# Kernel tuning notes

Hardware: AMD Instinct MI355X
Metric: run time of the kernel (lower is better)

Reference implementation:

```python
import jax, jax.numpy as jnp
import numpy as np

V, E, H = 50257, 512, 1024  # vocab, embed_dim, hidden_dim
B, S = 64, 2048             # batch, src_len


def setup_inputs() -> dict:
    key = jax.random.key(0)
    ks = jax.random.split(key, 16)
    sc = 0.02
    emb = jax.random.normal(ks[0], (V, E), jnp.float32) * sc
    emb = emb.at[0].set(0.0)  # padding_idx=0
    return {
        "x": jax.random.randint(ks[1], (B, 1), 0, V),
        "hidden": jax.random.normal(ks[2], (1, B, H), jnp.float32),
        "cell": jax.random.normal(ks[3], (1, B, H), jnp.float32),
        "encoder_outputs": jax.random.normal(ks[4], (B, S, H), jnp.float32),
        "emb": emb,
        "Wa_w": jax.random.normal(ks[5], (H, H), jnp.float32) * sc,
        "Wa_b": jnp.zeros((H,), jnp.float32),
        "Ua_w": jax.random.normal(ks[6], (H, H), jnp.float32) * sc,
        "Ua_b": jnp.zeros((H,), jnp.float32),
        "va_w": jax.random.normal(ks[7], (1, H), jnp.float32) * sc,
        "va_b": jnp.zeros((1,), jnp.float32),
        "Wih": jax.random.normal(ks[8], (4 * H, E + H), jnp.float32) * sc,
        "Whh": jax.random.normal(ks[9], (4 * H, H), jnp.float32) * sc,
        "bih": jnp.zeros((4 * H,), jnp.float32),
        "bhh": jnp.zeros((4 * H,), jnp.float32),
        "fc_w": jax.random.normal(ks[10], (V, H), jnp.float32) * sc,
        "fc_b": jnp.zeros((V,), jnp.float32),
    }


def reference(x, hidden, cell, encoder_outputs, emb, Wa_w, Wa_b, Ua_w, Ua_b,
              va_w, va_b, Wih, Whh, bih, bhh, fc_w, fc_b):
    # Embedding lookup: [B,1] -> [B,E]
    embedded = emb[x[:, 0]]
    # Bahdanau additive attention
    s_t = hidden[-1]                                          # [B,H]
    proj_s = jnp.einsum('bh,oh->bo', s_t, Wa_w) + Wa_b        # [B,H]
    proj_e = jnp.einsum('bsh,oh->bso', encoder_outputs, Ua_w) + Ua_b  # [B,S,H]
    e = jnp.tanh(proj_s[:, None, :] + proj_e)                 # [B,S,H]
    scores = jnp.einsum('bsh,h->bs', e, va_w[0]) + va_b[0]    # [B,S]
    attn = jax.nn.softmax(scores, axis=1)                     # [B,S]
    context = jnp.einsum('bs,bsh->bh', attn, encoder_outputs)  # [B,H]
    # Single-step LSTM (torch gate order: i, f, g, o)
    lstm_in = jnp.concatenate([embedded, context], axis=1)    # [B,E+H]
    gates = lstm_in @ Wih.T + bih + s_t @ Whh.T + bhh         # [B,4H]
    i, f, g, o = jnp.split(gates, 4, axis=1)
    i, f, o = jax.nn.sigmoid(i), jax.nn.sigmoid(f), jax.nn.sigmoid(o)
    g = jnp.tanh(g)
    c_new = f * cell[-1] + i * g
    h_new = o * jnp.tanh(c_new)
    predictions = (h_new @ fc_w.T + fc_b)[:, None, :]          # [B,1,V]
    return predictions, h_new[None], c_new[None]
```

## Files before the change

### kernel.cpp

```cpp
#include <hip/hip_runtime.h>
#include <hip/hip_bf16.h>

#define V_ 50257
#define H_ 1024
#define S_ 2048

typedef float f32x4 __attribute__((ext_vector_type(4)));
typedef short s16x8 __attribute__((ext_vector_type(8)));

__device__ __forceinline__ unsigned short f2bf(float f){
  unsigned u = __builtin_bit_cast(unsigned, f);
  return (unsigned short)((u + 0x7FFFu + ((u >> 16) & 1u)) >> 16);
}
__device__ __forceinline__ unsigned cvt2(float a, float b){
  return (unsigned)f2bf(a) | ((unsigned)f2bf(b) << 16);
}
__device__ __forceinline__ float bf2f(unsigned short h){
  return __builtin_bit_cast(float, (unsigned)h << 16);
}
__device__ __forceinline__ float fast_tanh(float x){
  return 1.0f - 2.0f/(__expf(2.0f*x)+1.0f);
}
__device__ __forceinline__ float fast_sig(float x){
  return 1.0f/(1.0f+__expf(-x));
}
__device__ __forceinline__ void gld_lds16(const void* g, void* l){
  __builtin_amdgcn_global_load_lds((const __attribute__((address_space(1))) void*)g,
                                   (__attribute__((address_space(3))) void*)l, 16, 0, 0);
}

#define BAR() do { __builtin_amdgcn_sched_barrier(0); __builtin_amdgcn_s_barrier(); __builtin_amdgcn_sched_barrier(0); } while(0)
#define VMW4() asm volatile("s_waitcnt vmcnt(4)" ::: "memory")
#define VMW2() asm volatile("s_waitcnt vmcnt(2)" ::: "memory")
#define VMW0() asm volatile("s_waitcnt vmcnt(0)" ::: "memory")

__global__ __launch_bounds__(256) void k_cvt_bf16(const float* __restrict__ src,
                                                  unsigned short* __restrict__ dst, int n){
  int i = (blockIdx.x*256 + threadIdx.x)*4;
  if (i < n){
    float4 f = *(const float4*)(src + i);
    uint2 u;
    u.x = cvt2(f.x, f.y);
    u.y = cvt2(f.z, f.w);
    *(uint2*)(dst + i) = u;
  }
}

__global__ __launch_bounds__(256) void k_cvt_enc(const float* __restrict__ src,
                                                 unsigned short* __restrict__ dst){
  const size_t stride = (size_t)gridDim.x * 256;
  const float4* s4 = (const float4*)src;
  uint2* d2 = (uint2*)dst;
  for (size_t i = (size_t)blockIdx.x*256 + threadIdx.x; i < 33554432u; i += stride){
    float4 f = s4[i];
    uint2 u;
    u.x = cvt2(f.x, f.y);
    u.y = cvt2(f.z, f.w);
    d2[i] = u;
  }
}

__global__ __launch_bounds__(1024,4) void k_proje256(
    const unsigned short* __restrict__ A,
    const unsigned short* __restrict__ Bw,
    const float* __restrict__ ps,
    const float* __restrict__ Ua_b,
    const float* __restrict__ va,
    float* __restrict__ part)
{
  extern __shared__ unsigned short smem[];
  const int t = threadIdx.x;
  const int lane = t & 63, wid = t >> 6;
  const int lr = lane & 15, lk = lane >> 4;
  const int wr = wid >> 2, wc = wid & 3;

  int bid = blockIdx.x;
  int L = (bid & 7) * 256 + (bid >> 3);
  const int wgm = L >> 2, wgn = L & 3;
  const int m0 = wgm * 256, n0 = wgn * 256;

  const int srow = lane >> 3;
  const int schunk = (lane & 7) ^ srow;

  f32x4 acc[4][4] = {};
  s16x8 af[4], bfr[4];

  auto STAGE_A = [&](int slot, int kt){
    #pragma unroll
    for (int h = 0; h < 2; ++h){
      unsigned short* ldst = smem + slot*16384;
      int rb = h*128 + wid*8;
      gld_lds16(A + (size_t)(m0 + rb + srow)*1024 + kt*64 + schunk*8,
                ldst + rb*64);
    }
  };
  auto STAGE_B = [&](int slot, int kt){
    #pragma unroll
    for (int h = 0; h < 2; ++h){
      unsigned short* ldst = smem + 32768 + slot*16384;
      int rb = h*128 + wid*8;
      gld_lds16(Bw + (size_t)(n0 + rb + srow)*1024 + kt*64 + schunk*8,
                ldst + rb*64);
    }
  };

#define SUBPH(As_, Bs_, ks) do { \
    _Pragma("unroll") \
    for (int ni = 0; ni < 4; ++ni){ \
      int rl = wc*64 + ni*16 + lr; \
      bfr[ni] = *(const s16x8*)((Bs_) + rl*64 + ((((ks)*4+lk) ^ (lr&7))*8)); \
    } \
    _Pragma("unroll") \
    for (int mi = 0; mi < 4; ++mi){ \
      int rl = wr*64 + mi*16 + lr; \
      af[mi] = *(const s16x8*)((As_) + rl*64 + ((((ks)*4+lk) ^ (lr&7))*8)); \
    } \
    __builtin_amdgcn_s_setprio(1); \
    _Pragma("unroll") \
    for (int mi = 0; mi < 4; ++mi) \
      _Pragma("unroll") \
      for (int ni = 0; ni < 4; ++ni) \
        acc[mi][ni] = __builtin_amdgcn_mfma_f32_16x16x32_bf16(af[mi], bfr[ni], acc[mi][ni], 0,0,0); \
    __builtin_amdgcn_s_setprio(0); \
  } while(0)

  const unsigned short* As0 = smem;
  const unsigned short* Bs0 = smem + 32768;
  const unsigned short* As1 = smem + 16384;
  const unsigned short* Bs1 = smem + 32768 + 16384;

  STAGE_A(0, 0); STAGE_B(0, 0);
  STAGE_A(1, 1); STAGE_B(1, 1);
  VMW4(); BAR();

  for (int i = 0; i < 8; ++i){
    SUBPH(As0, Bs0, 0);
    SUBPH(As0, Bs0, 1);
    BAR();
    if (i < 7){
      STAGE_A(0, 2*i + 2);
      VMW2(); BAR();
      SUBPH(As1, Bs1, 0);
      STAGE_B(0, 2*i + 2);
      SUBPH(As1, Bs1, 1);
      BAR();
      STAGE_A(1, 2*i + 3);
      STAGE_B(1, 2*i + 3);
      VMW4(); BAR();
    } else {
      VMW0(); BAR();
      SUBPH(As1, Bs1, 0);
      SUBPH(As1, Bs1, 1);
    }
  }

  const int b = m0 >> 11;
  float psv[4], vav[4];
  #pragma unroll
  for (int ni = 0; ni < 4; ++ni){
    int n = n0 + wc*64 + ni*16 + lr;
    psv[ni] = ps[b*1024 + n] + Ua_b[n];
    vav[ni] = va[n];
  }
  #pragma unroll
  for (int mi = 0; mi < 4; ++mi){
    float p0=0.f,p1=0.f,p2=0.f,p3=0.f;
    #pragma unroll
    for (int ni = 0; ni < 4; ++ni){
      p0 += vav[ni]*fast_tanh(acc[mi][ni][0] + psv[ni]);
      p1 += vav[ni]*fast_tanh(acc[mi][ni][1] + psv[ni]);
      p2 += vav[ni]*fast_tanh(acc[mi][ni][2] + psv[ni]);
      p3 += vav[ni]*fast_tanh(acc[mi][ni][3] + psv[ni]);
    }
    #pragma unroll
    for (int off = 1; off < 16; off <<= 1){
      p0 += __shfl_xor(p0, off);
      p1 += __shfl_xor(p1, off);
      p2 += __shfl_xor(p2, off);
      p3 += __shfl_xor(p3, off);
    }
    if (lr == 0){
      int rg = m0 + wr*64 + mi*16 + lk*4;
      int slot = wgn*4 + wc;
      part[(size_t)rg*16 + slot]     = p0;
      part[(size_t)(rg+1)*16 + slot] = p1;
      part[(size_t)(rg+2)*16 + slot] = p2;
      part[(size_t)(rg+3)*16 + slot] = p3;
    }
  }
#undef SUBPH
}

__global__ __launch_bounds__(256,2) void k_proje_f32(
    const float* __restrict__ A,
    const unsigned short* __restrict__ Bw,
    const float* __restrict__ ps,
    const float* __restrict__ Ua_b,
    const float* __restrict__ va,
    float* __restrict__ part)
{
  __shared__ unsigned char sm[32768];
  const int t = threadIdx.x;
  const int lane = t & 63, wid = t >> 6;
  const int lr = lane & 15, lk = lane >> 4;
  int bid = blockIdx.x;
  int L = (bid & 7) * 1024 + (bid >> 3);
  const int wgm = L >> 3, wgn = L & 7;
  const int m0 = wgm * 128, n0 = wgn * 128;
  const int wm = wid >> 1, wn = wid & 1;

  f32x4 acc[4][4] = {};
  const int row2 = t >> 1, half = t & 1;
  const float* aSrc = A + (size_t)(m0 + row2) * 1024 + half * 32;
  const unsigned short* bSrc = Bw + (size_t)(n0 + row2) * 1024 + half * 32;
  unsigned char* Al = sm;
  unsigned char* Bl = sm + 16384;
  const int swzr = row2 & 7;

  for (int kt = 0; kt < 16; ++kt){
    __syncthreads();
    #pragma unroll
    for (int c = 0; c < 4; ++c){
      float4 f0 = *(const float4*)(aSrc + kt*64 + c*8);
      float4 f1 = *(const float4*)(aSrc + kt*64 + c*8 + 4);
      union { unsigned u[4]; s16x8 v; } p;
      p.u[0]=cvt2(f0.x,f0.y); p.u[1]=cvt2(f0.z,f0.w);
      p.u[2]=cvt2(f1.x,f1.y); p.u[3]=cvt2(f1.z,f1.w);
      int ch = half*4 + c;
      *(s16x8*)(Al + row2*128 + ((ch ^ swzr)*16)) = p.v;
    }
    #pragma unroll
    for (int c = 0; c < 4; ++c){
      s16x8 v = *(const s16x8*)(bSrc + kt*64 + (half*4 + c)*8);
      *(s16x8*)(Bl + row2*128 + (((half*4+c) ^ swzr)*16)) = v;
    }
    __syncthreads();
    #pragma unroll
    for (int ks = 0; ks < 2; ++ks){
      s16x8 af[4], bfr[4];
      #pragma unroll
      for (int mi = 0; mi < 4; ++mi){
        int r = wm*64 + mi*16 + lr;
        af[mi] = *(const s16x8*)(Al + r*128 + (((ks*4+lk) ^ (lr&7))*16));
      }
      #pragma unroll
      for (int ni = 0; ni < 4; ++ni){
        int r = wn*64 + ni*16 + lr;
        bfr[ni] = *(const s16x8*)(Bl + r*128 + (((ks*4+lk) ^ (lr&7))*16));
      }
      #pragma unroll
      for (int mi = 0; mi < 4; ++mi)
        #pragma unroll
        for (int ni = 0; ni < 4; ++ni)
          acc[mi][ni] = __builtin_amdgcn_mfma_f32_16x16x32_bf16(af[mi], bfr[ni], acc[mi][ni], 0,0,0);
    }
  }
  const int b = m0 >> 11;
  float psv[4], vav[4];
  #pragma unroll
  for (int ni = 0; ni < 4; ++ni){
    int n = n0 + wn*64 + ni*16 + lr;
    psv[ni] = ps[b*1024 + n] + Ua_b[n];
    vav[ni] = va[n];
  }
  #pragma unroll
  for (int mi = 0; mi < 4; ++mi){
    float p0=0.f,p1=0.f,p2=0.f,p3=0.f;
    #pragma unroll
    for (int ni = 0; ni < 4; ++ni){
      p0 += vav[ni]*fast_tanh(acc[mi][ni][0] + psv[ni]);
      p1 += vav[ni]*fast_tanh(acc[mi][ni][1] + psv[ni]);
      p2 += vav[ni]*fast_tanh(acc[mi][ni][2] + psv[ni]);
      p3 += vav[ni]*fast_tanh(acc[mi][ni][3] + psv[ni]);
    }
    #pragma unroll
    for (int off = 1; off < 16; off <<= 1){
      p0 += __shfl_xor(p0, off);
      p1 += __shfl_xor(p1, off);
      p2 += __shfl_xor(p2, off);
      p3 += __shfl_xor(p3, off);
    }
    if (lr == 0){
      int rg = m0 + wm*64 + mi*16 + lk*4;
      int slot = wgn*2 + wn;
      part[(size_t)rg*16 + slot]     = p0;
      part[(size_t)(rg+1)*16 + slot] = p1;
      part[(size_t)(rg+2)*16 + slot] = p2;
      part[(size_t)(rg+3)*16 + slot] = p3;
    }
  }
}

__global__ __launch_bounds__(256,2) void k_gemm64(
    const float* __restrict__ A,
    const float* __restrict__ B1,
    const float* __restrict__ B2,
    const float* __restrict__ bias1,
    const float* __restrict__ bias2,
    float* __restrict__ C, int ldC,
    int N, int K, int K1)
{
  __shared__ unsigned char sm[16384];
  const int t = threadIdx.x;
  const int lane = t & 63, wid = t >> 6;
  const int lr = lane & 15, lk = lane >> 4;
  const int n0 = blockIdx.x * 64;
  f32x4 acc[4] = {};
  const int row = t >> 2, seg = t & 3;
  unsigned char* Al = sm;
  unsigned char* Bl = sm + 8192;
  const int swzr = row & 7;
  const int K2 = K - K1;

  for (int k0 = 0; k0 < K; k0 += 64){
    __syncthreads();
    {
      const float* s = A + (size_t)row*K + k0 + seg*16;
      #pragma unroll
      for (int c = 0; c < 2; ++c){
        float4 f0 = *(const float4*)(s + c*8);
        float4 f1 = *(const float4*)(s + c*8 + 4);
        union { unsigned u[4]; s16x8 v; } p;
        p.u[0]=cvt2(f0.x,f0.y); p.u[1]=cvt2(f0.z,f0.w);
        p.u[2]=cvt2(f1.x,f1.y); p.u[3]=cvt2(f1.z,f1.w);
        *(s16x8*)(Al + row*128 + (((seg*2+c) ^ swzr)*16)) = p.v;
      }
    }
    {
      int n = n0 + row;
      #pragma unroll
      for (int c = 0; c < 2; ++c){
        union { unsigned u[4]; s16x8 v; } p;
        if (n < N){
          int k = k0 + seg*16 + c*8;
          const float* s;
          if (k < K1) s = B1 + (size_t)n*K1 + k;
          else        s = B2 + (size_t)n*K2 + (k - K1);
          float4 f0 = *(const float4*)(s);
          float4 f1 = *(const float4*)(s + 4);
          p.u[0]=cvt2(f0.x,f0.y); p.u[1]=cvt2(f0.z,f0.w);
          p.u[2]=cvt2(f1.x,f1.y); p.u[3]=cvt2(f1.z,f1.w);
        } else {
          p.u[0]=0u; p.u[1]=0u; p.u[2]=0u; p.u[3]=0u;
        }
        *(s16x8*)(Bl + row*128 + (((seg*2+c) ^ swzr)*16)) = p.v;
      }
    }
    __syncthreads();
    #pragma unroll
    for (int ks = 0; ks < 2; ++ks){
      s16x8 bfr = *(const s16x8*)(Bl + (wid*16+lr)*128 + (((ks*4+lk) ^ (lr&7))*16));
      #pragma unroll
      for (int mi = 0; mi < 4; ++mi){
        s16x8 af = *(const s16x8*)(Al + (mi*16+lr)*128 + (((ks*4+lk) ^ (lr&7))*16));
        acc[mi] = __builtin_amdgcn_mfma_f32_16x16x32_bf16(af, bfr, acc[mi], 0,0,0);
      }
    }
  }
  int n = n0 + wid*16 + lr;
  if (n < N){
    float bv = (bias1 ? bias1[n] : 0.f) + (bias2 ? bias2[n] : 0.f);
    #pragma unroll
    for (int mi = 0; mi < 4; ++mi){
      #pragma unroll
      for (int r = 0; r < 4; ++r){
        C[(size_t)(mi*16 + lk*4 + r)*ldC + n] = acc[mi][r] + bv;
      }
    }
  }
}

__global__ __launch_bounds__(256,3) void k_gemm64b(
    const unsigned short* __restrict__ A,
    const float* __restrict__ B1,
    const float* __restrict__ B2,
    const float* __restrict__ bias1,
    const float* __restrict__ bias2,
    float* __restrict__ C, int ldC,
    int N, int K, int K1)
{
  __shared__ unsigned char sm[16384];
  const int t = threadIdx.x;
  const int lane = t & 63, wid = t >> 6;
  const int lr = lane & 15, lk = lane >> 4;
  const int n0 = blockIdx.x * 64;
  f32x4 acc[4] = {};
  const int row = t >> 2, seg = t & 3;
  unsigned char* Al = sm;
  unsigned char* Bl = sm + 8192;
  const int swzr = row & 7;
  const int K2 = K - K1;

  for (int k0 = 0; k0 < K; k0 += 64){
    __syncthreads();
    {
      const unsigned short* s = A + (size_t)row*K + k0 + seg*16;
      #pragma unroll
      for (int c = 0; c < 2; ++c){
        s16x8 v = *(const s16x8*)(s + c*8);
        *(s16x8*)(Al + row*128 + (((seg*2+c) ^ swzr)*16)) = v;
      }
    }
    {
      int n = n0 + row;
      #pragma unroll
      for (int c = 0; c < 2; ++c){
        union { unsigned u[4]; s16x8 v; } p;
        if (n < N){
          int k = k0 + seg*16 + c*8;
          const float* s;
          if (k < K1) s = B1 + (size_t)n*K1 + k;
          else        s = B2 + (size_t)n*K2 + (k - K1);
          float4 f0 = *(const float4*)(s);
          float4 f1 = *(const float4*)(s + 4);
          p.u[0]=cvt2(f0.x,f0.y); p.u[1]=cvt2(f0.z,f0.w);
          p.u[2]=cvt2(f1.x,f1.y); p.u[3]=cvt2(f1.z,f1.w);
        } else {
          p.u[0]=0u; p.u[1]=0u; p.u[2]=0u; p.u[3]=0u;
        }
        *(s16x8*)(Bl + row*128 + (((seg*2+c) ^ swzr)*16)) = p.v;
      }
    }
    __syncthreads();
    #pragma unroll
    for (int ks = 0; ks < 2; ++ks){
      s16x8 bfr = *(const s16x8*)(Bl + (wid*16+lr)*128 + (((ks*4+lk) ^ (lr&7))*16));
      #pragma unroll
      for (int mi = 0; mi < 4; ++mi){
        s16x8 af = *(const s16x8*)(Al + (mi*16+lr)*128 + (((ks*4+lk) ^ (lr&7))*16));
        acc[mi] = __builtin_amdgcn_mfma_f32_16x16x32_bf16(af, bfr, acc[mi], 0,0,0);
      }
    }
  }
  int n = n0 + wid*16 + lr;
  if (n < N){
    float bv = (bias1 ? bias1[n] : 0.f) + (bias2 ? bias2[n] : 0.f);
    #pragma unroll
    for (int mi = 0; mi < 4; ++mi){
      #pragma unroll
      for (int r = 0; r < 4; ++r){
        C[(size_t)(mi*16 + lk*4 + r)*ldC + n] = acc[mi][r] + bv;
      }
    }
  }
}

__global__ __launch_bounds__(256) void k_softmax(const float* __restrict__ part,
                                                 const float* __restrict__ va_b,
                                                 float* __restrict__ attn){
  __shared__ float sc[2048];
  __shared__ float red[8];
  const int b = blockIdx.x, t = threadIdx.x;
  float vb = va_b[0];
  float lmax = -1e30f;
  #pragma unroll
  for (int j = 0; j < 8; ++j){
    int s = t + j*256;
    const float* p = part + ((size_t)b*2048 + s)*16;
    float v = vb;
    #pragma unroll
    for (int i = 0; i < 16; ++i) v += p[i];
    sc[s] = v;
    lmax = fmaxf(lmax, v);
  }
  for (int off = 32; off; off >>= 1) lmax = fmaxf(lmax, __shfl_xor(lmax, off));
  if ((t&63)==0) red[t>>6] = lmax;
  __syncthreads();
  float m = fmaxf(fmaxf(red[0],red[1]),fmaxf(red[2],red[3]));
  float lsum = 0.f;
  #pragma unroll
  for (int j = 0; j < 8; ++j){
    int s = t + j*256;
    float e = __expf(sc[s]-m);
    sc[s] = e; lsum += e;
  }
  for (int off = 32; off; off >>= 1) lsum += __shfl_xor(lsum, off);
  if ((t&63)==0) red[4 + (t>>6)] = lsum;
  __syncthreads();
  float inv = 1.f/(red[4]+red[5]+red[6]+red[7]);
  #pragma unroll
  for (int j = 0; j < 8; ++j){
    int s = t + j*256;
    attn[(size_t)b*2048+s] = sc[s]*inv;
  }
}

__global__ __launch_bounds__(256) void k_context_bf(const float* __restrict__ attn,
                                                    const unsigned short* __restrict__ encb,
                                                    float* __restrict__ ctxp){
  const int b = blockIdx.x >> 4, scid = blockIdx.x & 15;
  const int t = threadIdx.x;
  float a0=0.f,a1=0.f,a2=0.f,a3=0.f;
  const unsigned short* e = encb + ((size_t)b*2048 + scid*128)*1024 + t*4;
  const float* at = attn + (size_t)b*2048 + scid*128;
  #pragma unroll 4
  for (int s = 0; s < 128; ++s){
    float a = at[s];
    ushort4 v = *(const ushort4*)(e + (size_t)s*1024);
    a0 += a*bf2f(v.x); a1 += a*bf2f(v.y); a2 += a*bf2f(v.z); a3 += a*bf2f(v.w);
  }
  float4 o; o.x=a0; o.y=a1; o.z=a2; o.w=a3;
  *(float4*)(ctxp + ((size_t)scid*64 + b)*1024 + t*4) = o;
}

__global__ __launch_bounds__(256) void k_context_f32(const float* __restrict__ attn,
                                                     const float* __restrict__ enc,
                                                     float* __restrict__ ctxp){
  const int b = blockIdx.x >> 4, scid = blockIdx.x & 15;
  const int t = threadIdx.x;
  float a0=0.f,a1=0.f,a2=0.f,a3=0.f;
  const float* e = enc + ((size_t)b*2048 + scid*128)*1024;
  const float* at = attn + (size_t)b*2048 + scid*128;
  for (int s = 0; s < 128; ++s){
    float a = at[s];
    const float* er = e + (size_t)s*1024;
    a0 += a*er[t]; a1 += a*er[t+256]; a2 += a*er[t+512]; a3 += a*er[t+768];
  }
  float* o = ctxp + ((size_t)scid*64 + b)*1024;
  o[t]=a0; o[t+256]=a1; o[t+512]=a2; o[t+768]=a3;
}

__global__ __launch_bounds__(256) void k_build(const int* __restrict__ x,
                                               const float* __restrict__ emb,
                                               const float* __restrict__ ctxp,
                                               const float* __restrict__ hidden,
                                               unsigned short* __restrict__ lstm){
  const int b = blockIdx.x, t = threadIdx.x;
  int xe = x[b];
  for (int col = t; col < 2560; col += 256){
    float v;
    if (col < 512) v = emb[(size_t)xe*512 + col];
    else if (col < 1536){
      int h = col - 512;
      v = 0.f;
      #pragma unroll
      for (int i = 0; i < 16; ++i) v += ctxp[((size_t)i*64 + b)*1024 + h];
    } else v = hidden[(size_t)b*1024 + (col-1536)];
    lstm[(size_t)b*2560 + col] = f2bf(v);
  }
}

__global__ __launch_bounds__(256) void k_lstm(const float* __restrict__ gates,
                                              const float* __restrict__ cell,
                                              float* __restrict__ out,
                                              unsigned short* __restrict__ hbf){
  int idx = blockIdx.x*256 + threadIdx.x;
  int b = idx >> 10, h = idx & 1023;
  const float* g = gates + (size_t)b*4096;
  float gi = fast_sig(g[h]);
  float gf = fast_sig(g[h+1024]);
  float gg = fast_tanh(g[h+2048]);
  float go = fast_sig(g[h+3072]);
  float c  = gf*cell[idx] + gi*gg;
  float hn = go*fast_tanh(c);
  out[(size_t)V_*64 + idx]         = hn;
  out[(size_t)V_*64 + 65536 + idx] = c;
  hbf[idx] = f2bf(hn);
}

extern "C" void kernel_launch(void* const* d_in, const int* in_sizes, int n_in,
                              void* d_out, int out_size, void* d_ws, size_t ws_size,
                              hipStream_t stream){
  const int*   x     = (const int*)d_in[0];
  const float* hidden= (const float*)d_in[1];
  const float* cell  = (const float*)d_in[2];
  const float* enc   = (const float*)d_in[3];
  const float* emb   = (const float*)d_in[4];
  const float* Wa_w  = (const float*)d_in[5];
  const float* Wa_b  = (const float*)d_in[6];
  const float* Ua_w  = (const float*)d_in[7];
  const float* Ua_b  = (const float*)d_in[8];
  const float* va_w  = (const float*)d_in[9];
  const float* va_b  = (const float*)d_in[10];
  const float* Wih   = (const float*)d_in[11];
  const float* Whh   = (const float*)d_in[12];
  const float* bih   = (const float*)d_in[13];
  const float* bhh   = (const float*)d_in[14];
  const float* fc_w  = (const float*)d_in[15];
  const float* fc_b  = (const float*)d_in[16];
  float* out = (float*)d_out;
  char* ws = (char*)d_ws;
  unsigned short* ua_bf = (unsigned short*)(ws + 0);
  float* ps    = (float*)(ws + 2097152);
  float* attn  = (float*)(ws + 2359296);
  unsigned short* lstm_bf = (unsigned short*)(ws + 2883584);
  float* gates = (float*)(ws + 3538944);
  float* part  = (float*)(ws + 6684672);
  float* ctxp  = (float*)(ws + 10878976);
  unsigned short* h_bf = (unsigned short*)(ws + 15073280);
  unsigned short* enc_bf = (unsigned short*)(ws + 16777216);
  const size_t REQ = 16777216u + 268435456u;

  hipLaunchKernelGGL(k_cvt_bf16, dim3(1024), dim3(256), 0, stream, Ua_w, ua_bf, 1048576);
  hipLaunchKernelGGL(k_gemm64, dim3(16), dim3(256), 0, stream,
                     hidden, Wa_w, nullptr, Wa_b, nullptr, ps, 1024, 1024, 1024, 1024);
  if (ws_size >= REQ){
    hipLaunchKernelGGL(k_cvt_enc, dim3(8192), dim3(256), 0, stream, enc, enc_bf);
    hipLaunchKernelGGL(k_proje256, dim3(2048), dim3(1024), 131072, stream,
                       enc_bf, ua_bf, ps, Ua_b, va_w, part);
    hipLaunchKernelGGL(k_softmax, dim3(64), dim3(256), 0, stream, part, va_b, attn);
    hipLaunchKernelGGL(k_context_bf, dim3(1024), dim3(256), 0, stream, attn, enc_bf, ctxp);
  } else {
    hipLaunchKernelGGL(k_proje_f32, dim3(8192), dim3(256), 0, stream,
                       enc, ua_bf, ps, Ua_b, va_w, part);
    hipLaunchKernelGGL(k_softmax, dim3(64), dim3(256), 0, stream, part, va_b, attn);
    hipLaunchKernelGGL(k_context_f32, dim3(1024), dim3(256), 0, stream, attn, enc, ctxp);
  }
  hipLaunchKernelGGL(k_build, dim3(64), dim3(256), 0, stream, x, emb, ctxp, hidden, lstm_bf);
  hipLaunchKernelGGL(k_gemm64b, dim3(64), dim3(256), 0, stream,
                     lstm_bf, Wih, Whh, bih, bhh, gates, 4096, 4096, 2560, 1536);
  hipLaunchKernelGGL(k_lstm, dim3(256), dim3(256), 0, stream, gates, cell, out, h_bf);
  hipLaunchKernelGGL(k_gemm64b, dim3(786), dim3(256), 0, stream,
                     h_bf, fc_w, nullptr, fc_b, nullptr, out, V_, V_, 1024, 1024);
}
```

Baseline: 646.6 us.

## Restructure proj_e GEMM staging into 4-slot K=32 pipeline with single barrier

```diff
diff --git a/kernel.cpp b/kernel.cpp
--- a/kernel.cpp
+++ b/kernel.cpp
@@ -79,41 +79,31 @@
   const int wgm = L >> 2, wgn = L & 3;
   const int m0 = wgm * 256, n0 = wgn * 256;
 
-  const int srow = lane >> 3;
-  const int schunk = (lane & 7) ^ srow;
+  const int srow = wid*16 + (lane >> 2);
+  const int schunk = (lane & 3) ^ ((lane >> 2) & 3);
 
   f32x4 acc[4][4] = {};
   s16x8 af[4], bfr[4];
 
-  auto STAGE_A = [&](int slot, int kt){
-    #pragma unroll
-    for (int h = 0; h < 2; ++h){
-      unsigned short* ldst = smem + slot*16384;
-      int rb = h*128 + wid*8;
-      gld_lds16(A + (size_t)(m0 + rb + srow)*1024 + kt*64 + schunk*8,
-                ldst + rb*64);
-    }
+  auto STAGE = [&](int slot, int kt){
+    unsigned short* ldstA = smem + slot*8192 + wid*512;
+    unsigned short* ldstB = smem + 32768 + slot*8192 + wid*512;
+    gld_lds16(A  + (size_t)(m0 + srow)*1024 + kt*32 + schunk*8, ldstA);
+    gld_lds16(Bw + (size_t)(n0 + srow)*1024 + kt*32 + schunk*8, ldstB);
   };
-  auto STAGE_B = [&](int slot, int kt){
-    #pragma unroll
-    for (int h = 0; h < 2; ++h){
-      unsigned short* ldst = smem + 32768 + slot*16384;
-      int rb = h*128 + wid*8;
-      gld_lds16(Bw + (size_t)(n0 + rb + srow)*1024 + kt*64 + schunk*8,
-                ldst + rb*64);
-    }
-  };
-
-#define SUBPH(As_, Bs_, ks) do { \
+
+#define COMPUTE(slot) do { \
+    const unsigned short* As_ = smem + (slot)*8192; \
+    const unsigned short* Bs_ = smem + 32768 + (slot)*8192; \
     _Pragma("unroll") \
     for (int ni = 0; ni < 4; ++ni){ \
       int rl = wc*64 + ni*16 + lr; \
-      bfr[ni] = *(const s16x8*)((Bs_) + rl*64 + ((((ks)*4+lk) ^ (lr&7))*8)); \
+      bfr[ni] = *(const s16x8*)(Bs_ + rl*32 + ((lk ^ (lr&3))*8)); \
     } \
     _Pragma("unroll") \
     for (int mi = 0; mi < 4; ++mi){ \
       int rl = wr*64 + mi*16 + lr; \
-      af[mi] = *(const s16x8*)((As_) + rl*64 + ((((ks)*4+lk) ^ (lr&7))*8)); \
+      af[mi] = *(const s16x8*)(As_ + rl*32 + ((lk ^ (lr&3))*8)); \
     } \
     __builtin_amdgcn_s_setprio(1); \
     _Pragma("unroll") \
@@ -124,35 +114,17 @@
     __builtin_amdgcn_s_setprio(0); \
   } while(0)
 
-  const unsigned short* As0 = smem;
-  const unsigned short* Bs0 = smem + 32768;
-  const unsigned short* As1 = smem + 16384;
-  const unsigned short* Bs1 = smem + 32768 + 16384;
-
-  STAGE_A(0, 0); STAGE_B(0, 0);
-  STAGE_A(1, 1); STAGE_B(1, 1);
-  VMW4(); BAR();
-
-  for (int i = 0; i < 8; ++i){
-    SUBPH(As0, Bs0, 0);
-    SUBPH(As0, Bs0, 1);
+  STAGE(0, 0); STAGE(1, 1); STAGE(2, 2);
+
+  for (int tt = 0; tt < 29; ++tt){
+    VMW4();
     BAR();
-    if (i < 7){
-      STAGE_A(0, 2*i + 2);
-      VMW2(); BAR();
-      SUBPH(As1, Bs1, 0);
-      STAGE_B(0, 2*i + 2);
-      SUBPH(As1, Bs1, 1);
-      BAR();
-      STAGE_A(1, 2*i + 3);
-      STAGE_B(1, 2*i + 3);
-      VMW4(); BAR();
-    } else {
-      VMW0(); BAR();
-      SUBPH(As1, Bs1, 0);
-      SUBPH(As1, Bs1, 1);
-    }
-  }
+    COMPUTE(tt & 3);
+    STAGE((tt + 3) & 3, tt + 3);
+  }
+  VMW4(); BAR(); COMPUTE(29 & 3);
+  VMW2(); BAR(); COMPUTE(30 & 3);
+  VMW0(); BAR(); COMPUTE(31 & 3);
 
   const int b = m0 >> 11;
   float psv[4], vav[4];
@@ -188,7 +160,7 @@
       part[(size_t)(rg+3)*16 + slot] = p3;
     }
   }
-#undef SUBPH
+#undef COMPUTE
 }
 
 __global__ __launch_bounds__(256,2) void k_proje_f32(
```

Result: slower. 663.0 us (+2.5%).
